# Kernel optimization log

Hardware: AMD Instinct MI355X
Metric: run time of the kernel (lower is better)

Reference implementation:

```python
import jax, jax.numpy as jnp
import numpy as np

B, S, D, H, W = 8, 2048, 128, 8, 64
INT_HEADS = 8          # hardcoded in SpatioTemporalLayer1
EPS_COS = 1e-8
EPS_LN = 1e-5


def _mha(q_in, k_in, v_in, in_w, in_b, out_w, out_b, nh, mask=None):
    # q_in/k_in/v_in: (batch, len, d); torch nn.MultiheadAttention math (eval, no dropout)
    b, lq, d = q_in.shape
    hd = d // nh
    q = (q_in @ in_w[:d].T + in_b[:d]).reshape(b, lq, nh, hd)
    k = (k_in @ in_w[d:2 * d].T + in_b[d:2 * d]).reshape(b, k_in.shape[1], nh, hd)
    v = (v_in @ in_w[2 * d:].T + in_b[2 * d:]).reshape(b, v_in.shape[1], nh, hd)
    scores = jnp.einsum('bihd,bjhd->bhij', q, k) / jnp.sqrt(jnp.asarray(hd, q_in.dtype))
    if mask is not None:
        scores = scores + mask
    attn = jax.nn.softmax(scores, axis=-1)
    out = jnp.einsum('bhij,bjhd->bihd', attn, v).reshape(b, lq, d)
    return out @ out_w.T + out_b


def _layernorm(x, g, b):
    mu = x.mean(-1, keepdims=True)
    var = ((x - mu) ** 2).mean(-1, keepdims=True)
    return (x - mu) * jax.lax.rsqrt(var + EPS_LN) * g + b


def _cos_normalize(e):
    n = jnp.maximum(jnp.linalg.norm(e, axis=-1, keepdims=True), EPS_COS)
    return e / n


def _forward(x, spatial_info, temporal_info,
             lw_in_w, lw_in_b, lw_out_w, lw_out_b,
             spat_w, spat_b, temp_w, temp_b,
             int_in_w, int_in_b, int_out_w, int_out_b,
             ffn_w1, ffn_b1, ffn_w2, ffn_b2,
             ln1_g, ln1_b, ln2_g, ln2_b):
    b, s, d = x.shape
    # --- local window attention (S % W == 0 here, so no padding path) ---
    nw = s // W
    xw = x.reshape(b * nw, W, d)
    causal = jnp.triu(jnp.full((W, W), -jnp.inf, x.dtype), k=1)
    attn = _mha(xw, xw, xw, lw_in_w, lw_in_b, lw_out_w, lw_out_b, H, causal).reshape(b, s, d)
    x = _layernorm(attn + x, ln1_g, ln1_b)
    # --- FFN (torch nn.GELU default = exact erf) ---
    h = jax.nn.gelu(x @ ffn_w1.T + ffn_b1, approximate=False)
    x = _layernorm(h @ ffn_w2.T + ffn_b2 + x, ln2_g, ln2_b)
    # --- spatio-temporal interaction ---
    se = spatial_info @ spat_w.T + spat_b
    te = temporal_info @ temp_w.T + temp_b
    sn = _cos_normalize(se)
    tn = _cos_normalize(te)
    ss = jnp.einsum('bid,bjd->bij', sn, sn)   # (B,S,S) spatial cosine sim
    ts = jnp.einsum('bid,bjd->bij', tn, tn)   # (B,S,S) temporal cosine sim
    # interaction MHA is batch_first=False: it treats (B,S,D) as (len=B, batch=S, d).
    # Equivalent batch-first call on swapped axes (faithful to the torch source).
    inter = jnp.swapaxes(
        _mha(jnp.swapaxes(se, 0, 1), jnp.swapaxes(te, 0, 1), jnp.swapaxes(te, 0, 1),
             int_in_w, int_in_b, int_out_w, int_out_b, INT_HEADS), 0, 1)
    # similarity[b,i,j,d] = ss[b,i,j]*ts[b,i,j]*inter[b,i,d]; mean over j factorizes:
    sim = (ss * ts).mean(axis=2)              # (B,S)
    return x + sim[..., None] * inter


def setup_inputs() -> dict:
    key = jax.random.key(0)
    ks = jax.random.split(key, 24)
    sc = 0.02
    inp = {
        'x': jax.random.normal(ks[0], (B, S, D), jnp.float32),
        'spatial_info': jax.random.normal(ks[1], (B, S, D), jnp.float32),
        'temporal_info': jax.random.normal(ks[2], (B, S, D), jnp.float32),
        'lw_in_w': jax.random.normal(ks[3], (3 * D, D), jnp.float32) * sc,
        'lw_in_b': jnp.zeros((3 * D,), jnp.float32),
        'lw_out_w': jax.random.normal(ks[4], (D, D), jnp.float32) * sc,
        'lw_out_b': jnp.zeros((D,), jnp.float32),
        'spat_w': jax.random.normal(ks[5], (D, D), jnp.float32) * sc,
        'spat_b': jnp.zeros((D,), jnp.float32),
        'temp_w': jax.random.normal(ks[6], (D, D), jnp.float32) * sc,
        'temp_b': jnp.zeros((D,), jnp.float32),
        'int_in_w': jax.random.normal(ks[7], (3 * D, D), jnp.float32) * sc,
        'int_in_b': jnp.zeros((3 * D,), jnp.float32),
        'int_out_w': jax.random.normal(ks[8], (D, D), jnp.float32) * sc,
        'int_out_b': jnp.zeros((D,), jnp.float32),
        'ffn_w1': jax.random.normal(ks[9], (4 * D, D), jnp.float32) * sc,
        'ffn_b1': jnp.zeros((4 * D,), jnp.float32),
        'ffn_w2': jax.random.normal(ks[10], (D, 4 * D), jnp.float32) * sc,
        'ffn_b2': jnp.zeros((D,), jnp.float32),
        'ln1_g': jnp.ones((D,), jnp.float32),
        'ln1_b': jnp.zeros((D,), jnp.float32),
        'ln2_g': jnp.ones((D,), jnp.float32),
        'ln2_b': jnp.zeros((D,), jnp.float32),
    }
    return inp


def reference(x, spatial_info, temporal_info,
              lw_in_w, lw_in_b, lw_out_w, lw_out_b,
              spat_w, spat_b, temp_w, temp_b,
              int_in_w, int_in_b, int_out_w, int_out_b,
              ffn_w1, ffn_b1, ffn_w2, ffn_b2,
              ln1_g, ln1_b, ln2_g, ln2_b):
    return _forward(x, spatial_info, temporal_info,
                    lw_in_w, lw_in_b, lw_out_w, lw_out_b,
                    spat_w, spat_b, temp_w, temp_b,
                    int_in_w, int_in_b, int_out_w, int_out_b,
                    ffn_w1, ffn_b1, ffn_w2, ffn_b2,
                    ln1_g, ln1_b, ln2_g, ln2_b)
```

## Files before the change

kernel.cpp:

```cpp
#include <hip/hip_runtime.h>
#include <math.h>

#define BB 8
#define SS 2048
#define NTOK (BB * SS)
#define ATB_SPLIT 16

using bf16x8 = __attribute__((ext_vector_type(8))) short;
using f32x4  = __attribute__((ext_vector_type(4))) float;

__device__ __forceinline__ float gelu_tanh(float x) {
    float y = 0.7978845608f * (x + 0.044715f * x * x * x);
    float e = __expf(2.0f * y);
    float t = 1.0f - 2.0f / (e + 1.0f);
    return 0.5f * x * (1.0f + t);
}
__device__ __forceinline__ unsigned short f2b(float f) {
    unsigned int u = __float_as_uint(f);
    u += 0x7FFFu + ((u >> 16) & 1u);
    return (unsigned short)(u >> 16);
}
__device__ __forceinline__ float b2f(unsigned short u) {
    return __uint_as_float((unsigned int)u << 16);
}
__device__ __forceinline__ bf16x8 ldg_f32_b8(const float* p) {
    float4 f0 = *(const float4*)p, f1 = *(const float4*)(p + 4);
    union { ushort4 u[2]; bf16x8 v; } r;
    r.u[0] = (ushort4){f2b(f0.x), f2b(f0.y), f2b(f0.z), f2b(f0.w)};
    r.u[1] = (ushort4){f2b(f1.x), f2b(f1.y), f2b(f1.z), f2b(f1.w)};
    return r.v;
}

__global__ __launch_bounds__(256) void phaseA(
    const float* __restrict__ x,
    const float* __restrict__ lw_in_w, const float* __restrict__ b_in,
    const float* __restrict__ lw_out_w, const float* __restrict__ b_out,
    const float* __restrict__ lng, const float* __restrict__ lnb,
    float* __restrict__ x1, unsigned short* __restrict__ x1b,
    const float* __restrict__ ffn_w1, const float* __restrict__ ffn_w2,
    unsigned short* __restrict__ Wb)
{
    __shared__ unsigned short Qs[64 * 136];
    __shared__ unsigned short Ks[64 * 136];
    __shared__ unsigned short Vt[128 * 72];
    __shared__ unsigned short Pb[4][32 * 72];
    __shared__ float red[2][64][2];
    const int tid = threadIdx.x;

    if (blockIdx.x >= 256) {
        int i = (blockIdx.x - 256) * 256 + tid;
        float v = (i < 65536) ? ffn_w1[i] : ffn_w2[i - 65536];
        Wb[i] = f2b(v);
        return;
    }

    const int m0 = blockIdx.x * 64;
    const int wv = tid >> 6, lane = tid & 63, ln = lane & 15, q = lane >> 4;
    const int wm = (wv >> 1) * 32, wn = (wv & 1) * 64;

    bf16x8 afr[4][2];
    #pragma unroll
    for (int kf = 0; kf < 4; ++kf)
        #pragma unroll
        for (int fm = 0; fm < 2; ++fm)
            afr[kf][fm] = ldg_f32_b8(x + (size_t)(m0 + wm + fm * 16 + ln) * 128 + kf * 32 + q * 8);

    #pragma unroll
    for (int p = 0; p < 3; ++p) {
        f32x4 acc[2][4] = {};
        #pragma unroll
        for (int kf = 0; kf < 4; ++kf) {
            bf16x8 b[4];
            #pragma unroll
            for (int fn = 0; fn < 4; ++fn)
                b[fn] = ldg_f32_b8(lw_in_w + (size_t)(p * 128 + wn + fn * 16 + ln) * 128 + kf * 32 + q * 8);
            #pragma unroll
            for (int fm = 0; fm < 2; ++fm)
                #pragma unroll
                for (int fn = 0; fn < 4; ++fn)
                    acc[fm][fn] = __builtin_amdgcn_mfma_f32_16x16x32_bf16(afr[kf][fm], b[fn], acc[fm][fn], 0, 0, 0);
        }
        #pragma unroll
        for (int fm = 0; fm < 2; ++fm)
            #pragma unroll
            for (int r = 0; r < 4; ++r) {
                int rl = wm + fm * 16 + q * 4 + r;
                #pragma unroll
                for (int fn = 0; fn < 4; ++fn) {
                    int col = wn + fn * 16 + ln;
                    unsigned short v = f2b(acc[fm][fn][r] + b_in[p * 128 + col]);
                    if (p == 0)      Qs[rl * 136 + col] = v;
                    else if (p == 1) Ks[rl * 136 + col] = v;
                    else             Vt[col * 72 + rl] = v;
                }
            }
    }
    __syncthreads();

    {
        const int mh = wv >> 1, hq = wv & 1;
        unsigned short* P = &Pb[wv][0];
        #pragma unroll
        for (int hh = 0; hh < 4; ++hh) {
            const int h = hq * 4 + hh;
            f32x4 sacc[2][4] = {};
            bf16x8 az[2] = {}, bz[4] = {};
            if (q < 2) {
                #pragma unroll
                for (int fm = 0; fm < 2; ++fm)
                    az[fm] = *(const bf16x8*)&Qs[(mh * 32 + fm * 16 + ln) * 136 + h * 16 + q * 8];
                #pragma unroll
                for (int fn = 0; fn < 4; ++fn)
                    bz[fn] = *(const bf16x8*)&Ks[(fn * 16 + ln) * 136 + h * 16 + q * 8];
            }
            #pragma unroll
            for (int fm = 0; fm < 2; ++fm)
                #pragma unroll
                for (int fn = 0; fn < 4; ++fn)
                    sacc[fm][fn] = __builtin_amdgcn_mfma_f32_16x16x32_bf16(az[fm], bz[fn], sacc[fm][fn], 0, 0, 0);
            float invr[2][4];
            #pragma unroll
            for (int fm = 0; fm < 2; ++fm)
                #pragma unroll
                for (int r = 0; r < 4; ++r) {
                    int gi = mh * 32 + fm * 16 + q * 4 + r;
                    float mx = -1e30f;
                    #pragma unroll
                    for (int fn = 0; fn < 4; ++fn) {
                        int j = fn * 16 + ln;
                        float s = sacc[fm][fn][r] * 0.25f;
                        if (j > gi) s = -1e30f;
                        sacc[fm][fn][r] = s;
                        mx = fmaxf(mx, s);
                    }
                    #pragma unroll
                    for (int off = 1; off < 16; off <<= 1)
                        mx = fmaxf(mx, __shfl_xor(mx, off, 64));
                    float sum = 0.0f;
                    #pragma unroll
                    for (int fn = 0; fn < 4; ++fn) {
                        float p_ = __expf(sacc[fm][fn][r] - mx);
                        sacc[fm][fn][r] = p_;
                        sum += p_;
                    }
                    #pragma unroll
                    for (int off = 1; off < 16; off <<= 1)
                        sum += __shfl_xor(sum, off, 64);
                    invr[fm][r] = 1.0f / sum;
                    #pragma unroll
                    for (int fn = 0; fn < 4; ++fn)
                        P[(fm * 16 + q * 4 + r) * 72 + fn * 16 + ln] = f2b(sacc[fm][fn][r]);
                }
            f32x4 oacc[2] = {};
            #pragma unroll
            for (int kf2 = 0; kf2 < 2; ++kf2) {
                bf16x8 pa[2], vb;
                #pragma unroll
                for (int fm = 0; fm < 2; ++fm)
                    pa[fm] = *(const bf16x8*)&P[(fm * 16 + ln) * 72 + kf2 * 32 + q * 8];
                vb = *(const bf16x8*)&Vt[(h * 16 + ln) * 72 + kf2 * 32 + q * 8];
                #pragma unroll
                for (int fm = 0; fm < 2; ++fm)
                    oacc[fm] = __builtin_amdgcn_mfma_f32_16x16x32_bf16(pa[fm], vb, oacc[fm], 0, 0, 0);
            }
            #pragma unroll
            for (int fm = 0; fm < 2; ++fm)
                #pragma unroll
                for (int r = 0; r < 4; ++r)
                    Qs[(mh * 32 + fm * 16 + q * 4 + r) * 136 + h * 16 + ln] =
                        f2b(oacc[fm][r] * invr[fm][r]);
        }
    }
    __syncthreads();

    f32x4 acc[2][4] = {};
    #pragma unroll
    for (int kf = 0; kf < 4; ++kf) {
        bf16x8 a[2], b[4];
        #pragma unroll
        for (int fm = 0; fm < 2; ++fm)
            a[fm] = *(const bf16x8*)&Qs[(wm + fm * 16 + ln) * 136 + kf * 32 + q * 8];
        #pragma unroll
        for (int fn = 0; fn < 4; ++fn)
            b[fn] = ldg_f32_b8(lw_out_w + (size_t)(wn + fn * 16 + ln) * 128 + kf * 32 + q * 8);
        #pragma unroll
        for (int fm = 0; fm < 2; ++fm)
            #pragma unroll
            for (int fn = 0; fn < 4; ++fn)
                acc[fm][fn] = __builtin_amdgcn_mfma_f32_16x16x32_bf16(a[fm], b[fn], acc[fm][fn], 0, 0, 0);
    }
    #pragma unroll
    for (int fm = 0; fm < 2; ++fm)
        #pragma unroll
        for (int r = 0; r < 4; ++r) {
            int rl = wm + fm * 16 + q * 4 + r;
            int row = m0 + rl;
            float s1 = 0.0f, s2 = 0.0f;
            #pragma unroll
            for (int fn = 0; fn < 4; ++fn) {
                int col = wn + fn * 16 + ln;
                float vv = acc[fm][fn][r] + b_out[col] + x[(size_t)row * 128 + col];
                acc[fm][fn][r] = vv;
                s1 += vv; s2 += vv * vv;
            }
            #pragma unroll
            for (int off = 1; off < 16; off <<= 1) {
                s1 += __shfl_xor(s1, off, 64);
                s2 += __shfl_xor(s2, off, 64);
            }
            if (ln == 0) { red[0][rl][wv & 1] = s1; red[1][rl][wv & 1] = s2; }
        }
    __syncthreads();
    #pragma unroll
    for (int fm = 0; fm < 2; ++fm)
        #pragma unroll
        for (int r = 0; r < 4; ++r) {
            int rl = wm + fm * 16 + q * 4 + r;
            int row = m0 + rl;
            float mu = (red[0][rl][0] + red[0][rl][1]) * (1.0f / 128.0f);
            float var = (red[1][rl][0] + red[1][rl][1]) * (1.0f / 128.0f) - mu * mu;
            float rs = rsqrtf(var + 1e-5f);
            #pragma unroll
            for (int fn = 0; fn < 4; ++fn) {
                int col = wn + fn * 16 + ln;
                float o = (acc[fm][fn][r] - mu) * rs * lng[col] + lnb[col];
                x1[(size_t)row * 128 + col] = o;
                x1b[(size_t)row * 128 + col] = f2b(o);
            }
        }
}

__global__ __launch_bounds__(256) void phaseB(
    const unsigned short* __restrict__ x1b, const float* __restrict__ x1,
    const unsigned short* __restrict__ Wb,
    const float* __restrict__ b1, const float* __restrict__ b2,
    const float* __restrict__ lng, const float* __restrict__ lnb,
    float* __restrict__ x2,
    const float* __restrict__ spatial, const float* __restrict__ temporal,
    const float* __restrict__ spat_w, const float* __restrict__ temp_w,
    const float* __restrict__ bsp, const float* __restrict__ btp,
    unsigned short* __restrict__ snb, unsigned short* __restrict__ tnb,
    unsigned short* __restrict__ seb, unsigned short* __restrict__ teb)
{
    __shared__ unsigned short Xs[32 * 136];
    __shared__ unsigned short Hs[32 * 72];
    __shared__ float redf[2][32][2];
    __shared__ float redp[64][2];
    const int tid = threadIdx.x;
    const int wv = tid >> 6, lane = tid & 63, ln = lane & 15, q = lane >> 4;

    if (blockIdx.x < 512) {
        const int t0 = blockIdx.x * 32;
        const int wm = (wv >> 1) * 16;
        const int wn1 = (wv & 1) * 32, wn2 = (wv & 1) * 64;
        const unsigned short* w1 = Wb;
        const unsigned short* w2 = Wb + 65536;

        const uint4* X4 = (const uint4*)(x1b + (size_t)t0 * 128);
        #pragma unroll
        for (int t = 0; t < 2; ++t) {
            int idx = tid + t * 256;
            int r = idx >> 4, c = idx & 15;
            *(uint4*)&Xs[r * 136 + c * 8] = X4[r * 16 + c];
        }
        __syncthreads();
        bf16x8 xfr[4];
        #pragma unroll
        for (int kf = 0; kf < 4; ++kf)
            xfr[kf] = *(const bf16x8*)&Xs[(wm + ln) * 136 + kf * 32 + q * 8];

        f32x4 acc2[4] = {};
        for (int ch = 0; ch < 8; ++ch) {
            const int hc0 = ch * 64;
            f32x4 acc1[2] = {};
            #pragma unroll
            for (int kf = 0; kf < 4; ++kf) {
                #pragma unroll
                for (int fn = 0; fn < 2; ++fn) {
                    bf16x8 bb = *(const bf16x8*)&w1[(size_t)(hc0 + wn1 + fn * 16 + ln) * 128 + kf * 32 + q * 8];
                    acc1[fn] = __builtin_amdgcn_mfma_f32_16x16x32_bf16(xfr[kf], bb, acc1[fn], 0, 0, 0);
                }
            }
            #pragma unroll
            for (int fn = 0; fn < 2; ++fn)
                #pragma unroll
                for (int r = 0; r < 4; ++r) {
                    int rl = wm + q * 4 + r;
                    int col = wn1 + fn * 16 + ln;
                    Hs[rl * 72 + col] = f2b(gelu_tanh(acc1[fn][r] + b1[hc0 + col]));
                }
            __syncthreads();
            #pragma unroll
            for (int kf2 = 0; kf2 < 2; ++kf2) {
                bf16x8 a = *(const bf16x8*)&Hs[(wm + ln) * 72 + kf2 * 32 + q * 8];
                #pragma unroll
                for (int fn = 0; fn < 4; ++fn) {
                    bf16x8 bb = *(const bf16x8*)&w2[(size_t)(wn2 + fn * 16 + ln) * 512 + hc0 + kf2 * 32 + q * 8];
                    acc2[fn] = __builtin_amdgcn_mfma_f32_16x16x32_bf16(a, bb, acc2[fn], 0, 0, 0);
                }
            }
            __syncthreads();
        }
        #pragma unroll
        for (int r = 0; r < 4; ++r) {
            int rl = wm + q * 4 + r;
            int row = t0 + rl;
            float s1 = 0.0f, s2 = 0.0f;
            #pragma unroll
            for (int fn = 0; fn < 4; ++fn) {
                int col = wn2 + fn * 16 + ln;
                float vv = acc2[fn][r] + b2[col] + x1[(size_t)row * 128 + col];
                acc2[fn][r] = vv;
                s1 += vv; s2 += vv * vv;
            }
            #pragma unroll
            for (int off = 1; off < 16; off <<= 1) {
                s1 += __shfl_xor(s1, off, 64);
                s2 += __shfl_xor(s2, off, 64);
            }
            if (ln == 0) { redf[0][rl][wv & 1] = s1; redf[1][rl][wv & 1] = s2; }
        }
        __syncthreads();
        #pragma unroll
        for (int r = 0; r < 4; ++r) {
            int rl = wm + q * 4 + r;
            int row = t0 + rl;
            float mu = (redf[0][rl][0] + redf[0][rl][1]) * (1.0f / 128.0f);
            float var = (redf[1][rl][0] + redf[1][rl][1]) * (1.0f / 128.0f) - mu * mu;
            float rs = rsqrtf(var + 1e-5f);
            #pragma unroll
            for (int fn = 0; fn < 4; ++fn) {
                int col = wn2 + fn * 16 + ln;
                x2[(size_t)row * 128 + col] = (acc2[fn][r] - mu) * rs * lng[col] + lnb[col];
            }
        }
        return;
    }

    {
        const int idx2 = blockIdx.x - 512;
        const int y = idx2 >> 8;
        const int m0 = (idx2 & 255) * 64;
        const float* Af = y ? temporal : spatial;
        const float* Wf = y ? temp_w : spat_w;
        const float* bias = y ? btp : bsp;
        unsigned short* nb = y ? tnb : snb;
        unsigned short* raw = y ? teb : seb;
        const int wm = (wv >> 1) * 32, wn = (wv & 1) * 64;

        f32x4 acc[2][4] = {};
        #pragma unroll
        for (int kf = 0; kf < 4; ++kf) {
            bf16x8 a[2], b[4];
            #pragma unroll
            for (int fm = 0; fm < 2; ++fm)
                a[fm] = ldg_f32_b8(Af + (size_t)(m0 + wm + fm * 16 + ln) * 128 + kf * 32 + q * 8);
            #pragma unroll
            for (int fn = 0; fn < 4; ++fn)
                b[fn] = ldg_f32_b8(Wf + (size_t)(wn + fn * 16 + ln) * 128 + kf * 32 + q * 8);
            #pragma unroll
            for (int fm = 0; fm < 2; ++fm)
                #pragma unroll
                for (int fn = 0; fn < 4; ++fn)
                    acc[fm][fn] = __builtin_amdgcn_mfma_f32_16x16x32_bf16(a[fm], b[fn], acc[fm][fn], 0, 0, 0);
        }
        #pragma unroll
        for (int fm = 0; fm < 2; ++fm)
            #pragma unroll
            for (int r = 0; r < 4; ++r) {
                int rl = wm + fm * 16 + q * 4 + r;
                float s2 = 0.0f;
                #pragma unroll
                for (int fn = 0; fn < 4; ++fn) {
                    int col = wn + fn * 16 + ln;
                    float vv = acc[fm][fn][r] + bias[col];
                    acc[fm][fn][r] = vv;
                    s2 += vv * vv;
                }
                #pragma unroll
                for (int off = 1; off < 16; off <<= 1) s2 += __shfl_xor(s2, off, 64);
                if (ln == 0) redp[rl][wv & 1] = s2;
            }
        __syncthreads();
        #pragma unroll
        for (int fm = 0; fm < 2; ++fm)
            #pragma unroll
            for (int r = 0; r < 4; ++r) {
                int rl = wm + fm * 16 + q * 4 + r;
                int row = m0 + rl;
                float inv = 1.0f / fmaxf(sqrtf(redp[rl][0] + redp[rl][1]), 1e-8f);
                #pragma unroll
                for (int fn = 0; fn < 4; ++fn) {
                    int col = wn + fn * 16 + ln;
                    float vv = acc[fm][fn][r];
                    nb[(size_t)row * 128 + col] = f2b(vv * inv);
                    raw[(size_t)row * 128 + col] = f2b(vv);
                }
            }
    }
}

__global__ __launch_bounds__(256) void atb_split_kernel(
    const unsigned short* __restrict__ snb, const unsigned short* __restrict__ tnb,
    float* __restrict__ part)
{
    const int b = blockIdx.z / ATB_SPLIT;
    const int chunk = blockIdx.z % ATB_SPLIT;
    const int d0 = blockIdx.x * 64, e0 = blockIdx.y * 64;
    __shared__ float Ss[32][68];
    __shared__ float Ts[32][68];
    const int tid = threadIdx.x;
    const int tx = tid % 16, ty = tid / 16;
    const int jbase = chunk * (SS / ATB_SPLIT);
    float acc[4][4] = {};
    for (int j0 = jbase; j0 < jbase + SS / ATB_SPLIT; j0 += 32) {
        {
            int r = tid >> 3, c8 = (tid & 7) * 8;
            uint4 sv = *(const uint4*)&snb[(size_t)(b * SS + j0 + r) * 128 + d0 + c8];
            uint4 tv = *(const uint4*)&tnb[(size_t)(b * SS + j0 + r) * 128 + e0 + c8];
            const unsigned short* sp = (const unsigned short*)&sv;
            const unsigned short* tp = (const unsigned short*)&tv;
            #pragma unroll
            for (int c = 0; c < 8; ++c) {
                Ss[r][c8 + c] = b2f(sp[c]);
                Ts[r][c8 + c] = b2f(tp[c]);
            }
        }
        __syncthreads();
        #pragma unroll
        for (int kk = 0; kk < 32; ++kk) {
            float4 af = *(const float4*)&Ss[kk][ty * 4];
            float4 wf = *(const float4*)&Ts[kk][tx * 4];
            float a[4] = {af.x, af.y, af.z, af.w};
            float w[4] = {wf.x, wf.y, wf.z, wf.w};
            #pragma unroll
            for (int i = 0; i < 4; ++i)
                #pragma unroll
                for (int j = 0; j < 4; ++j)
                    acc[i][j] = fmaf(a[i], w[j], acc[i][j]);
        }
        __syncthreads();
    }
    float* pp = part + (size_t)(b * ATB_SPLIT + chunk) * 16384;
    #pragma unroll
    for (int i = 0; i < 4; ++i) {
        float4 ov = {acc[i][0], acc[i][1], acc[i][2], acc[i][3]};
        *(float4*)&pp[(size_t)(d0 + ty * 4 + i) * 128 + e0 + tx * 4] = ov;
    }
}

__global__ __launch_bounds__(256) void atb_reduce_kernel(
    const float* __restrict__ part, unsigned short* __restrict__ Mtb)
{
    int i = blockIdx.x * 256 + threadIdx.x;
    int b = i >> 14, rem = i & 16383;
    int e = rem >> 7, d = rem & 127;
    const float* pp = part + (size_t)b * ATB_SPLIT * 16384 + (size_t)d * 128 + e;
    float s = 0.0f;
    #pragma unroll
    for (int c = 0; c < ATB_SPLIT; ++c) s += pp[(size_t)c * 16384];
    Mtb[i] = f2b(s);
}

__global__ __launch_bounds__(256) void simgemm_kernel(
    const unsigned short* __restrict__ snb, const unsigned short* __restrict__ tnb,
    const unsigned short* __restrict__ Mtb, float* __restrict__ sim)
{
    __shared__ float red[64][2];
    const int tid = threadIdx.x, m0 = blockIdx.x * 64, b = m0 >> 11;
    const int wv = tid >> 6, lane = tid & 63, ln = lane & 15, q = lane >> 4;
    const int wm = (wv >> 1) * 32, wn = (wv & 1) * 64;

    f32x4 acc[2][4] = {};
    #pragma unroll
    for (int kf = 0; kf < 4; ++kf) {
        bf16x8 a[2], bb[4];
        #pragma unroll
        for (int fm = 0; fm < 2; ++fm)
            a[fm] = *(const bf16x8*)&snb[(size_t)(m0 + wm + fm * 16 + ln) * 128 + kf * 32 + q * 8];
        #pragma unroll
        for (int fn = 0; fn < 4; ++fn)
            bb[fn] = *(const bf16x8*)&Mtb[(size_t)b * 16384 + (size_t)(wn + fn * 16 + ln) * 128 + kf * 32 + q * 8];
        #pragma unroll
        for (int fm = 0; fm < 2; ++fm)
            #pragma unroll
            for (int fn = 0; fn < 4; ++fn)
                acc[fm][fn] = __builtin_amdgcn_mfma_f32_16x16x32_bf16(a[fm], bb[fn], acc[fm][fn], 0, 0, 0);
    }
    #pragma unroll
    for (int fm = 0; fm < 2; ++fm)
        #pragma unroll
        for (int r = 0; r < 4; ++r) {
            int rl = wm + fm * 16 + q * 4 + r;
            int row = m0 + rl;
            float s = 0.0f;
            #pragma unroll
            for (int fn = 0; fn < 4; ++fn) {
                int col = wn + fn * 16 + ln;
                s += acc[fm][fn][r] * b2f(tnb[(size_t)row * 128 + col]);
            }
            #pragma unroll
            for (int off = 1; off < 16; off <<= 1) s += __shfl_xor(s, off, 64);
            if (ln == 0) red[rl][wv & 1] = s;
        }
    __syncthreads();
    if (tid < 64) sim[m0 + tid] = (red[tid][0] + red[tid][1]) * (1.0f / (float)SS);
}

__global__ __launch_bounds__(256) void inter_block(
    const unsigned short* __restrict__ seb, const unsigned short* __restrict__ teb,
    const float* __restrict__ Wint,
    const float* __restrict__ b_int,
    const float* __restrict__ Wio,
    const float* __restrict__ b_io,
    const float* __restrict__ sim, const float* __restrict__ x2,
    float* __restrict__ out)
{
    __shared__ unsigned short Qs[64 * 136];
    __shared__ unsigned short KVs[64 * 256];
    const int tid = threadIdx.x, s0 = blockIdx.x * 8;
    const int wv = tid >> 6, lane = tid & 63, ln = lane & 15, q = lane >> 4;
    const int wm = (wv >> 1) * 32, wn = (wv & 1) * 64;

    bf16x8 afr[4][2];
    #pragma unroll
    for (int kf = 0; kf < 4; ++kf)
        #pragma unroll
        for (int fm = 0; fm < 2; ++fm) {
            int rl = wm + fm * 16 + ln;
            size_t g = (size_t)(rl >> 3) * 2048 + s0 + (rl & 7);
            afr[kf][fm] = *(const bf16x8*)&seb[g * 128 + kf * 32 + q * 8];
        }

    #pragma unroll
    for (int p = 0; p < 3; ++p) {
        if (p == 1) {
            #pragma unroll
            for (int kf = 0; kf < 4; ++kf)
                #pragma unroll
                for (int fm = 0; fm < 2; ++fm) {
                    int rl = wm + fm * 16 + ln;
                    size_t g = (size_t)(rl >> 3) * 2048 + s0 + (rl & 7);
                    afr[kf][fm] = *(const bf16x8*)&teb[g * 128 + kf * 32 + q * 8];
                }
        }
        f32x4 acc[2][4] = {};
        #pragma unroll
        for (int kf = 0; kf < 4; ++kf) {
            bf16x8 b[4];
            #pragma unroll
            for (int fn = 0; fn < 4; ++fn)
                b[fn] = ldg_f32_b8(Wint + (size_t)(p * 128 + wn + fn * 16 + ln) * 128 + kf * 32 + q * 8);
            #pragma unroll
            for (int fm = 0; fm < 2; ++fm)
                #pragma unroll
                for (int fn = 0; fn < 4; ++fn)
                    acc[fm][fn] = __builtin_amdgcn_mfma_f32_16x16x32_bf16(afr[kf][fm], b[fn], acc[fm][fn], 0, 0, 0);
        }
        #pragma unroll
        for (int fm = 0; fm < 2; ++fm)
            #pragma unroll
            for (int r = 0; r < 4; ++r) {
                int rl = wm + fm * 16 + q * 4 + r;
                #pragma unroll
                for (int fn = 0; fn < 4; ++fn) {
                    int col = wn + fn * 16 + ln;
                    unsigned short v = f2b(acc[fm][fn][r] + b_int[p * 128 + col]);
                    if (p == 0) Qs[rl * 136 + col] = v;
                    else        KVs[rl * 256 + (p - 1) * 128 + col] = v;
                }
            }
        __syncthreads();
    }

    #pragma unroll
    for (int tt = 0; tt < 2; ++tt) {
        int task = tid + tt * 256;
        int ss = task >> 6, h = (task >> 3) & 7, i = task & 7;
        int rq = i * 8 + ss;
        float qr[16];
        {
            uint4 q0 = *(const uint4*)&Qs[rq * 136 + h * 16];
            uint4 q1 = *(const uint4*)&Qs[rq * 136 + h * 16 + 8];
            const unsigned short* p0 = (const unsigned short*)&q0;
            const unsigned short* p1 = (const unsigned short*)&q1;
            #pragma unroll
            for (int c = 0; c < 8; ++c) { qr[c] = b2f(p0[c]); qr[8 + c] = b2f(p1[c]); }
        }
        float sc[8];
        #pragma unroll
        for (int j = 0; j < 8; ++j) {
            uint4 k0 = *(const uint4*)&KVs[(j * 8 + ss) * 256 + h * 16];
            uint4 k1 = *(const uint4*)&KVs[(j * 8 + ss) * 256 + h * 16 + 8];
            const unsigned short* kp0 = (const unsigned short*)&k0;
            const unsigned short* kp1 = (const unsigned short*)&k1;
            float s = 0.0f;
            #pragma unroll
            for (int c = 0; c < 8; ++c) {
                s = fmaf(qr[c], b2f(kp0[c]), s);
                s = fmaf(qr[8 + c], b2f(kp1[c]), s);
            }
            sc[j] = s * 0.25f;
        }
        float mx = -1e30f;
        #pragma unroll
        for (int j = 0; j < 8; ++j) mx = fmaxf(mx, sc[j]);
        float pe[8], se = 0.0f;
        #pragma unroll
        for (int j = 0; j < 8; ++j) { pe[j] = __expf(sc[j] - mx); se += pe[j]; }
        float inv = 1.0f / se;
        float o[16] = {};
        #pragma unroll
        for (int j = 0; j < 8; ++j) {
            uint4 v0 = *(const uint4*)&KVs[(j * 8 + ss) * 256 + 128 + h * 16];
            uint4 v1 = *(const uint4*)&KVs[(j * 8 + ss) * 256 + 128 + h * 16 + 8];
            const unsigned short* vp0 = (const unsigned short*)&v0;
            const unsigned short* vp1 = (const unsigned short*)&v1;
            #pragma unroll
            for (int c = 0; c < 8; ++c) {
                o[c]     += pe[j] * b2f(vp0[c]);
                o[8 + c] += pe[j] * b2f(vp1[c]);
            }
        }
        ushort4 w0 = (ushort4){f2b(o[0]*inv),  f2b(o[1]*inv),  f2b(o[2]*inv),  f2b(o[3]*inv)};
        ushort4 w1 = (ushort4){f2b(o[4]*inv),  f2b(o[5]*inv),  f2b(o[6]*inv),  f2b(o[7]*inv)};
        ushort4 w2 = (ushort4){f2b(o[8]*inv),  f2b(o[9]*inv),  f2b(o[10]*inv), f2b(o[11]*inv)};
        ushort4 w3 = (ushort4){f2b(o[12]*inv), f2b(o[13]*inv), f2b(o[14]*inv), f2b(o[15]*inv)};
        *(ushort4*)&Qs[rq * 136 + h * 16]      = w0;
        *(ushort4*)&Qs[rq * 136 + h * 16 + 4]  = w1;
        *(ushort4*)&Qs[rq * 136 + h * 16 + 8]  = w2;
        *(ushort4*)&Qs[rq * 136 + h * 16 + 12] = w3;
    }
    __syncthreads();

    f32x4 acc[2][4] = {};
    #pragma unroll
    for (int kf = 0; kf < 4; ++kf) {
        bf16x8 a[2], b[4];
        #pragma unroll
        for (int fm = 0; fm < 2; ++fm)
            a[fm] = *(const bf16x8*)&Qs[(wm + fm * 16 + ln) * 136 + kf * 32 + q * 8];
        #pragma unroll
        for (int fn = 0; fn < 4; ++fn)
            b[fn] = ldg_f32_b8(Wio + (size_t)(wn + fn * 16 + ln) * 128 + kf * 32 + q * 8);
        #pragma unroll
        for (int fm = 0; fm < 2; ++fm)
            #pragma unroll
            for (int fn = 0; fn < 4; ++fn)
                acc[fm][fn] = __builtin_amdgcn_mfma_f32_16x16x32_bf16(a[fm], b[fn], acc[fm][fn], 0, 0, 0);
    }
    #pragma unroll
    for (int fm = 0; fm < 2; ++fm)
        #pragma unroll
        for (int r = 0; r < 4; ++r) {
            int rl = wm + fm * 16 + q * 4 + r;
            size_t g = (size_t)(rl >> 3) * 2048 + s0 + (rl & 7);
            float sc = sim[g];
            #pragma unroll
            for (int fn = 0; fn < 4; ++fn) {
                int col = wn + fn * 16 + ln;
                out[g * 128 + col] = (acc[fm][fn][r] + b_io[col]) * sc + x2[g * 128 + col];
            }
        }
}

extern "C" void kernel_launch(void* const* d_in, const int* in_sizes, int n_in,
                              void* d_out, int out_size, void* d_ws, size_t ws_size,
                              hipStream_t stream)
{
    const float* x        = (const float*)d_in[0];
    const float* spatial  = (const float*)d_in[1];
    const float* temporal = (const float*)d_in[2];
    const float* lw_in_w  = (const float*)d_in[3];
    const float* lw_in_b  = (const float*)d_in[4];
    const float* lw_out_w = (const float*)d_in[5];
    const float* lw_out_b = (const float*)d_in[6];
    const float* spat_w   = (const float*)d_in[7];
    const float* spat_b   = (const float*)d_in[8];
    const float* temp_w   = (const float*)d_in[9];
    const float* temp_b   = (const float*)d_in[10];
    const float* int_in_w = (const float*)d_in[11];
    const float* int_in_b = (const float*)d_in[12];
    const float* int_out_w= (const float*)d_in[13];
    const float* int_out_b= (const float*)d_in[14];
    const float* ffn_w1   = (const float*)d_in[15];
    const float* ffn_b1   = (const float*)d_in[16];
    const float* ffn_w2   = (const float*)d_in[17];
    const float* ffn_b2   = (const float*)d_in[18];
    const float* ln1_g    = (const float*)d_in[19];
    const float* ln1_b    = (const float*)d_in[20];
    const float* ln2_g    = (const float*)d_in[21];
    const float* ln2_b    = (const float*)d_in[22];
    float* out = (float*)d_out;

    char* base = (char*)d_ws;
    float*          x1   = (float*)(base + 0);
    unsigned short* x1b  = (unsigned short*)(base + 8388608);
    float*          x2   = (float*)(base + 12582912);
    unsigned short* snb  = (unsigned short*)(base + 20971520);
    unsigned short* tnb  = (unsigned short*)(base + 25165824);
    unsigned short* seb  = (unsigned short*)(base + 29360128);
    unsigned short* teb  = (unsigned short*)(base + 33554432);
    unsigned short* Mtb  = (unsigned short*)(base + 37748736);
    float*          simb = (float*)(base + 38010880);
    unsigned short* Wb   = (unsigned short*)(base + 38076416);
    float*          part = x1;

    phaseA<<<768, 256, 0, stream>>>(
        x, lw_in_w, lw_in_b, lw_out_w, lw_out_b, ln1_g, ln1_b, x1, x1b,
        ffn_w1, ffn_w2, Wb);
    phaseB<<<1024, 256, 0, stream>>>(
        x1b, x1, Wb, ffn_b1, ffn_b2, ln2_g, ln2_b, x2,
        spatial, temporal, spat_w, temp_w, spat_b, temp_b,
        snb, tnb, seb, teb);
    atb_split_kernel<<<dim3(2, 2, 8 * ATB_SPLIT), 256, 0, stream>>>(snb, tnb, part);
    atb_reduce_kernel<<<512, 256, 0, stream>>>(part, Mtb);
    simgemm_kernel<<<256, 256, 0, stream>>>(snb, tnb, Mtb, simb);
    inter_block<<<2048 / 8, 256, 0, stream>>>(
        seb, teb, int_in_w, int_in_b, int_out_w, int_out_b, simb, x2, out);
}
```

Before: 247.9 us.

## Give each wave full rows in phaseB to remove block barriers

phaseB's FFN and projection branches are restructured so that each wave owns 16 full rows across all 128 output columns. The per-wave GELU staging buffer then needs no __syncthreads, and the LayerNorm and L2-norm reductions finish within a wave via shuffles instead of a shared-memory cross-wave combine. Each block now covers 64 rows, so the FFN grid halves and the launch drops from 1024 to 768 blocks. The trade-off is more accumulator registers per wave (8 fragments instead of 4) and weight reads that are no longer split across waves, which may lower occupancy.

```diff
diff --git a/kernel.cpp b/kernel.cpp
--- a/kernel.cpp
+++ b/kernel.cpp
@@ -242,161 +242,121 @@
     unsigned short* __restrict__ snb, unsigned short* __restrict__ tnb,
     unsigned short* __restrict__ seb, unsigned short* __restrict__ teb)
 {
-    __shared__ unsigned short Xs[32 * 136];
-    __shared__ unsigned short Hs[32 * 72];
-    __shared__ float redf[2][32][2];
-    __shared__ float redp[64][2];
+    __shared__ unsigned short HsP[4][16 * 72];
     const int tid = threadIdx.x;
     const int wv = tid >> 6, lane = tid & 63, ln = lane & 15, q = lane >> 4;
 
-    if (blockIdx.x < 512) {
-        const int t0 = blockIdx.x * 32;
-        const int wm = (wv >> 1) * 16;
-        const int wn1 = (wv & 1) * 32, wn2 = (wv & 1) * 64;
+    if (blockIdx.x < 256) {
+        const int r0 = blockIdx.x * 64 + wv * 16;
         const unsigned short* w1 = Wb;
         const unsigned short* w2 = Wb + 65536;
-
-        const uint4* X4 = (const uint4*)(x1b + (size_t)t0 * 128);
-        #pragma unroll
-        for (int t = 0; t < 2; ++t) {
-            int idx = tid + t * 256;
-            int r = idx >> 4, c = idx & 15;
-            *(uint4*)&Xs[r * 136 + c * 8] = X4[r * 16 + c];
-        }
-        __syncthreads();
-        bf16x8 xfr[4];
+        unsigned short* Hp = &HsP[wv][0];
+
+        bf16x8 xa[4];
         #pragma unroll
         for (int kf = 0; kf < 4; ++kf)
-            xfr[kf] = *(const bf16x8*)&Xs[(wm + ln) * 136 + kf * 32 + q * 8];
-
-        f32x4 acc2[4] = {};
+            xa[kf] = *(const bf16x8*)&x1b[(size_t)(r0 + ln) * 128 + kf * 32 + q * 8];
+
+        f32x4 acc2[8] = {};
+        #pragma unroll
         for (int ch = 0; ch < 8; ++ch) {
             const int hc0 = ch * 64;
-            f32x4 acc1[2] = {};
-            #pragma unroll
-            for (int kf = 0; kf < 4; ++kf) {
-                #pragma unroll
-                for (int fn = 0; fn < 2; ++fn) {
-                    bf16x8 bb = *(const bf16x8*)&w1[(size_t)(hc0 + wn1 + fn * 16 + ln) * 128 + kf * 32 + q * 8];
-                    acc1[fn] = __builtin_amdgcn_mfma_f32_16x16x32_bf16(xfr[kf], bb, acc1[fn], 0, 0, 0);
+            f32x4 acc1[4] = {};
+            #pragma unroll
+            for (int kf = 0; kf < 4; ++kf)
+                #pragma unroll
+                for (int fn = 0; fn < 4; ++fn) {
+                    bf16x8 bb = *(const bf16x8*)&w1[(size_t)(hc0 + fn * 16 + ln) * 128 + kf * 32 + q * 8];
+                    acc1[fn] = __builtin_amdgcn_mfma_f32_16x16x32_bf16(xa[kf], bb, acc1[fn], 0, 0, 0);
                 }
-            }
-            #pragma unroll
-            for (int fn = 0; fn < 2; ++fn)
+            #pragma unroll
+            for (int fn = 0; fn < 4; ++fn)
                 #pragma unroll
                 for (int r = 0; r < 4; ++r) {
-                    int rl = wm + q * 4 + r;
-                    int col = wn1 + fn * 16 + ln;
-                    Hs[rl * 72 + col] = f2b(gelu_tanh(acc1[fn][r] + b1[hc0 + col]));
+                    int col = fn * 16 + ln;
+                    Hp[(q * 4 + r) * 72 + col] = f2b(gelu_tanh(acc1[fn][r] + b1[hc0 + col]));
                 }
-            __syncthreads();
             #pragma unroll
             for (int kf2 = 0; kf2 < 2; ++kf2) {
-                bf16x8 a = *(const bf16x8*)&Hs[(wm + ln) * 72 + kf2 * 32 + q * 8];
-                #pragma unroll
-                for (int fn = 0; fn < 4; ++fn) {
-                    bf16x8 bb = *(const bf16x8*)&w2[(size_t)(wn2 + fn * 16 + ln) * 512 + hc0 + kf2 * 32 + q * 8];
-                    acc2[fn] = __builtin_amdgcn_mfma_f32_16x16x32_bf16(a, bb, acc2[fn], 0, 0, 0);
+                bf16x8 ha = *(const bf16x8*)&Hp[ln * 72 + kf2 * 32 + q * 8];
+                #pragma unroll
+                for (int fn = 0; fn < 8; ++fn) {
+                    bf16x8 bb = *(const bf16x8*)&w2[(size_t)(fn * 16 + ln) * 512 + hc0 + kf2 * 32 + q * 8];
+                    acc2[fn] = __builtin_amdgcn_mfma_f32_16x16x32_bf16(ha, bb, acc2[fn], 0, 0, 0);
                 }
             }
-            __syncthreads();
         }
         #pragma unroll
         for (int r = 0; r < 4; ++r) {
-            int rl = wm + q * 4 + r;
-            int row = t0 + rl;
+            int row = r0 + q * 4 + r;
             float s1 = 0.0f, s2 = 0.0f;
-            #pragma unroll
-            for (int fn = 0; fn < 4; ++fn) {
-                int col = wn2 + fn * 16 + ln;
-                float vv = acc2[fn][r] + b2[col] + x1[(size_t)row * 128 + col];
-                acc2[fn][r] = vv;
-                s1 += vv; s2 += vv * vv;
+            float vv[8];
+            #pragma unroll
+            for (int fn = 0; fn < 8; ++fn) {
+                int col = fn * 16 + ln;
+                vv[fn] = acc2[fn][r] + b2[col] + x1[(size_t)row * 128 + col];
+                s1 += vv[fn]; s2 += vv[fn] * vv[fn];
             }
             #pragma unroll
             for (int off = 1; off < 16; off <<= 1) {
                 s1 += __shfl_xor(s1, off, 64);
                 s2 += __shfl_xor(s2, off, 64);
             }
-            if (ln == 0) { redf[0][rl][wv & 1] = s1; redf[1][rl][wv & 1] = s2; }
-        }
-        __syncthreads();
-        #pragma unroll
-        for (int r = 0; r < 4; ++r) {
-            int rl = wm + q * 4 + r;
-            int row = t0 + rl;
-            float mu = (redf[0][rl][0] + redf[0][rl][1]) * (1.0f / 128.0f);
-            float var = (redf[1][rl][0] + redf[1][rl][1]) * (1.0f / 128.0f) - mu * mu;
+            float mu = s1 * (1.0f / 128.0f);
+            float var = s2 * (1.0f / 128.0f) - mu * mu;
             float rs = rsqrtf(var + 1e-5f);
             #pragma unroll
-            for (int fn = 0; fn < 4; ++fn) {
-                int col = wn2 + fn * 16 + ln;
-                x2[(size_t)row * 128 + col] = (acc2[fn][r] - mu) * rs * lng[col] + lnb[col];
+            for (int fn = 0; fn < 8; ++fn) {
+                int col = fn * 16 + ln;
+                x2[(size_t)row * 128 + col] = (vv[fn] - mu) * rs * lng[col] + lnb[col];
             }
         }
         return;
     }
 
     {
-        const int idx2 = blockIdx.x - 512;
+        const int idx2 = blockIdx.x - 256;
         const int y = idx2 >> 8;
-        const int m0 = (idx2 & 255) * 64;
+        const int r0 = (idx2 & 255) * 64 + wv * 16;
         const float* Af = y ? temporal : spatial;
         const float* Wf = y ? temp_w : spat_w;
         const float* bias = y ? btp : bsp;
         unsigned short* nb = y ? tnb : snb;
         unsigned short* raw = y ? teb : seb;
-        const int wm = (wv >> 1) * 32, wn = (wv & 1) * 64;
-
-        f32x4 acc[2][4] = {};
-        #pragma unroll
-        for (int kf = 0; kf < 4; ++kf) {
-            bf16x8 a[2], b[4];
-            #pragma unroll
-            for (int fm = 0; fm < 2; ++fm)
-                a[fm] = ldg_f32_b8(Af + (size_t)(m0 + wm + fm * 16 + ln) * 128 + kf * 32 + q * 8);
-            #pragma unroll
-            for (int fn = 0; fn < 4; ++fn)
-                b[fn] = ldg_f32_b8(Wf + (size_t)(wn + fn * 16 + ln) * 128 + kf * 32 + q * 8);
-            #pragma unroll
-            for (int fm = 0; fm < 2; ++fm)
-                #pragma unroll
-                for (int fn = 0; fn < 4; ++fn)
-                    acc[fm][fn] = __builtin_amdgcn_mfma_f32_16x16x32_bf16(a[fm], b[fn], acc[fm][fn], 0, 0, 0);
-        }
-        #pragma unroll
-        for (int fm = 0; fm < 2; ++fm)
-            #pragma unroll
-            for (int r = 0; r < 4; ++r) {
-                int rl = wm + fm * 16 + q * 4 + r;
-                float s2 = 0.0f;
-                #pragma unroll
-                for (int fn = 0; fn < 4; ++fn) {
-                    int col = wn + fn * 16 + ln;
-                    float vv = acc[fm][fn][r] + bias[col];
-                    acc[fm][fn][r] = vv;
-                    s2 += vv * vv;
-                }
-                #pragma unroll
-                for (int off = 1; off < 16; off <<= 1) s2 += __shfl_xor(s2, off, 64);
-                if (ln == 0) redp[rl][wv & 1] = s2;
-            }
-        __syncthreads();
-        #pragma unroll
-        for (int fm = 0; fm < 2; ++fm)
-            #pragma unroll
-            for (int r = 0; r < 4; ++r) {
-                int rl = wm + fm * 16 + q * 4 + r;
-                int row = m0 + rl;
-                float inv = 1.0f / fmaxf(sqrtf(redp[rl][0] + redp[rl][1]), 1e-8f);
-                #pragma unroll
-                for (int fn = 0; fn < 4; ++fn) {
-                    int col = wn + fn * 16 + ln;
-                    float vv = acc[fm][fn][r];
-                    nb[(size_t)row * 128 + col] = f2b(vv * inv);
-                    raw[(size_t)row * 128 + col] = f2b(vv);
-                }
-            }
+
+        bf16x8 a[4];
+        #pragma unroll
+        for (int kf = 0; kf < 4; ++kf)
+            a[kf] = ldg_f32_b8(Af + (size_t)(r0 + ln) * 128 + kf * 32 + q * 8);
+
+        f32x4 acc[8] = {};
+        #pragma unroll
+        for (int kf = 0; kf < 4; ++kf)
+            #pragma unroll
+            for (int fn = 0; fn < 8; ++fn) {
+                bf16x8 bb = ldg_f32_b8(Wf + (size_t)(fn * 16 + ln) * 128 + kf * 32 + q * 8);
+                acc[fn] = __builtin_amdgcn_mfma_f32_16x16x32_bf16(a[kf], bb, acc[fn], 0, 0, 0);
+            }
+        #pragma unroll
+        for (int r = 0; r < 4; ++r) {
+            int row = r0 + q * 4 + r;
+            float s2 = 0.0f;
+            float vv[8];
+            #pragma unroll
+            for (int fn = 0; fn < 8; ++fn) {
+                vv[fn] = acc[fn][r] + bias[fn * 16 + ln];
+                s2 += vv[fn] * vv[fn];
+            }
+            #pragma unroll
+            for (int off = 1; off < 16; off <<= 1) s2 += __shfl_xor(s2, off, 64);
+            float inv = 1.0f / fmaxf(sqrtf(s2), 1e-8f);
+            #pragma unroll
+            for (int fn = 0; fn < 8; ++fn) {
+                int col = fn * 16 + ln;
+                nb[(size_t)row * 128 + col] = f2b(vv[fn] * inv);
+                raw[(size_t)row * 128 + col] = f2b(vv[fn]);
+            }
+        }
     }
 }
 
@@ -709,7 +669,7 @@
     phaseA<<<768, 256, 0, stream>>>(
         x, lw_in_w, lw_in_b, lw_out_w, lw_out_b, ln1_g, ln1_b, x1, x1b,
         ffn_w1, ffn_w2, Wb);
-    phaseB<<<1024, 256, 0, stream>>>(
+    phaseB<<<768, 256, 0, stream>>>(
         x1b, x1, Wb, ffn_b1, ffn_b2, ln2_g, ln2_b, x2,
         spatial, temporal, spat_w, temp_w, spat_b, temp_b,
         snb, tnb, seb, teb);
```

New measurement: 286.9 us. 1.16x slower.

## Split phaseB into separate FFN and projection kernels with larger FFN row tiles

Applied to the files above, without the earlier changes.

The combined phaseB kernel is split into a dedicated fused FFN kernel and a separate spatio-temporal projection kernel. The FFN kernel now processes 64 tokens per block instead of 32, so each W1/W2 fragment loaded from global memory feeds twice as many MFMAs. The hidden tile is double-buffered in shared memory, which removes the second barrier per chunk. In exchange the FFN grid drops to 256 blocks with higher register and LDS use, and there is one extra kernel launch.

```diff
diff --git a/kernel.cpp b/kernel.cpp
--- a/kernel.cpp
+++ b/kernel.cpp
@@ -230,174 +230,186 @@
         }
 }
 
-__global__ __launch_bounds__(256) void phaseB(
+__global__ __launch_bounds__(256) void ffn_fused(
     const unsigned short* __restrict__ x1b, const float* __restrict__ x1,
-    const unsigned short* __restrict__ Wb,
+    const unsigned short* __restrict__ w1, const unsigned short* __restrict__ w2,
     const float* __restrict__ b1, const float* __restrict__ b2,
     const float* __restrict__ lng, const float* __restrict__ lnb,
-    float* __restrict__ x2,
-    const float* __restrict__ spatial, const float* __restrict__ temporal,
-    const float* __restrict__ spat_w, const float* __restrict__ temp_w,
+    float* __restrict__ x2)
+{
+    __shared__ unsigned short Xs[64 * 136];
+    __shared__ unsigned short Hs[2][64 * 72];
+    __shared__ float red[2][64][2];
+    const int tid = threadIdx.x, t0 = blockIdx.x * 64;
+    const int wv = tid >> 6, lane = tid & 63, ln = lane & 15, q = lane >> 4;
+    const int wm = (wv >> 1) * 32;
+    const int wn1 = (wv & 1) * 32, wn2 = (wv & 1) * 64;
+
+    const uint4* X4 = (const uint4*)(x1b + (size_t)t0 * 128);
+    #pragma unroll
+    for (int t = 0; t < 4; ++t) {
+        int idx = tid + t * 256;
+        int r = idx >> 4, c = idx & 15;
+        *(uint4*)&Xs[r * 136 + c * 8] = X4[r * 16 + c];
+    }
+    __syncthreads();
+
+    bf16x8 xfr[4][2];
+    #pragma unroll
+    for (int kf = 0; kf < 4; ++kf)
+        #pragma unroll
+        for (int fm = 0; fm < 2; ++fm)
+            xfr[kf][fm] = *(const bf16x8*)&Xs[(wm + fm * 16 + ln) * 136 + kf * 32 + q * 8];
+
+    f32x4 acc2[2][4] = {};
+    for (int ch = 0; ch < 8; ++ch) {
+        const int hc0 = ch * 64;
+        unsigned short* Hb = &Hs[ch & 1][0];
+        f32x4 acc1[2][2] = {};
+        #pragma unroll
+        for (int kf = 0; kf < 4; ++kf) {
+            bf16x8 b[2];
+            #pragma unroll
+            for (int fn = 0; fn < 2; ++fn)
+                b[fn] = *(const bf16x8*)&w1[(size_t)(hc0 + wn1 + fn * 16 + ln) * 128 + kf * 32 + q * 8];
+            #pragma unroll
+            for (int fm = 0; fm < 2; ++fm)
+                #pragma unroll
+                for (int fn = 0; fn < 2; ++fn)
+                    acc1[fm][fn] = __builtin_amdgcn_mfma_f32_16x16x32_bf16(xfr[kf][fm], b[fn], acc1[fm][fn], 0, 0, 0);
+        }
+        #pragma unroll
+        for (int fm = 0; fm < 2; ++fm)
+            #pragma unroll
+            for (int fn = 0; fn < 2; ++fn)
+                #pragma unroll
+                for (int r = 0; r < 4; ++r) {
+                    int rl = wm + fm * 16 + q * 4 + r;
+                    int col = wn1 + fn * 16 + ln;
+                    Hb[rl * 72 + col] = f2b(gelu_tanh(acc1[fm][fn][r] + b1[hc0 + col]));
+                }
+        __syncthreads();
+        #pragma unroll
+        for (int kf2 = 0; kf2 < 2; ++kf2) {
+            bf16x8 a[2], b[4];
+            #pragma unroll
+            for (int fm = 0; fm < 2; ++fm)
+                a[fm] = *(const bf16x8*)&Hb[(wm + fm * 16 + ln) * 72 + kf2 * 32 + q * 8];
+            #pragma unroll
+            for (int fn = 0; fn < 4; ++fn)
+                b[fn] = *(const bf16x8*)&w2[(size_t)(wn2 + fn * 16 + ln) * 512 + hc0 + kf2 * 32 + q * 8];
+            #pragma unroll
+            for (int fm = 0; fm < 2; ++fm)
+                #pragma unroll
+                for (int fn = 0; fn < 4; ++fn)
+                    acc2[fm][fn] = __builtin_amdgcn_mfma_f32_16x16x32_bf16(a[fm], b[fn], acc2[fm][fn], 0, 0, 0);
+        }
+    }
+    #pragma unroll
+    for (int fm = 0; fm < 2; ++fm)
+        #pragma unroll
+        for (int r = 0; r < 4; ++r) {
+            int rl = wm + fm * 16 + q * 4 + r;
+            int row = t0 + rl;
+            float s1 = 0.0f, s2 = 0.0f;
+            #pragma unroll
+            for (int fn = 0; fn < 4; ++fn) {
+                int col = wn2 + fn * 16 + ln;
+                float vv = acc2[fm][fn][r] + b2[col] + x1[(size_t)row * 128 + col];
+                acc2[fm][fn][r] = vv;
+                s1 += vv; s2 += vv * vv;
+            }
+            #pragma unroll
+            for (int off = 1; off < 16; off <<= 1) {
+                s1 += __shfl_xor(s1, off, 64);
+                s2 += __shfl_xor(s2, off, 64);
+            }
+            if (ln == 0) { red[0][rl][wv & 1] = s1; red[1][rl][wv & 1] = s2; }
+        }
+    __syncthreads();
+    #pragma unroll
+    for (int fm = 0; fm < 2; ++fm)
+        #pragma unroll
+        for (int r = 0; r < 4; ++r) {
+            int rl = wm + fm * 16 + q * 4 + r;
+            int row = t0 + rl;
+            float mu = (red[0][rl][0] + red[0][rl][1]) * (1.0f / 128.0f);
+            float var = (red[1][rl][0] + red[1][rl][1]) * (1.0f / 128.0f) - mu * mu;
+            float rs = rsqrtf(var + 1e-5f);
+            #pragma unroll
+            for (int fn = 0; fn < 4; ++fn) {
+                int col = wn2 + fn * 16 + ln;
+                x2[(size_t)row * 128 + col] = (acc2[fm][fn][r] - mu) * rs * lng[col] + lnb[col];
+            }
+        }
+}
+
+__global__ __launch_bounds__(256) void stproj_kernel(
+    const float* __restrict__ sp, const float* __restrict__ tp,
+    const float* __restrict__ Wsp, const float* __restrict__ Wtp,
     const float* __restrict__ bsp, const float* __restrict__ btp,
     unsigned short* __restrict__ snb, unsigned short* __restrict__ tnb,
     unsigned short* __restrict__ seb, unsigned short* __restrict__ teb)
 {
-    __shared__ unsigned short Xs[32 * 136];
-    __shared__ unsigned short Hs[32 * 72];
-    __shared__ float redf[2][32][2];
-    __shared__ float redp[64][2];
-    const int tid = threadIdx.x;
+    __shared__ float red[64][2];
+    const int tid = threadIdx.x, m0 = blockIdx.x * 64, y = blockIdx.y;
+    const float* Af = y ? tp : sp;
+    const float* Wf = y ? Wtp : Wsp;
+    const float* bias = y ? btp : bsp;
+    unsigned short* nb = y ? tnb : snb;
+    unsigned short* raw = y ? teb : seb;
     const int wv = tid >> 6, lane = tid & 63, ln = lane & 15, q = lane >> 4;
-
-    if (blockIdx.x < 512) {
-        const int t0 = blockIdx.x * 32;
-        const int wm = (wv >> 1) * 16;
-        const int wn1 = (wv & 1) * 32, wn2 = (wv & 1) * 64;
-        const unsigned short* w1 = Wb;
-        const unsigned short* w2 = Wb + 65536;
-
-        const uint4* X4 = (const uint4*)(x1b + (size_t)t0 * 128);
-        #pragma unroll
-        for (int t = 0; t < 2; ++t) {
-            int idx = tid + t * 256;
-            int r = idx >> 4, c = idx & 15;
-            *(uint4*)&Xs[r * 136 + c * 8] = X4[r * 16 + c];
-        }
-        __syncthreads();
-        bf16x8 xfr[4];
-        #pragma unroll
-        for (int kf = 0; kf < 4; ++kf)
-            xfr[kf] = *(const bf16x8*)&Xs[(wm + ln) * 136 + kf * 32 + q * 8];
-
-        f32x4 acc2[4] = {};
-        for (int ch = 0; ch < 8; ++ch) {
-            const int hc0 = ch * 64;
-            f32x4 acc1[2] = {};
-            #pragma unroll
-            for (int kf = 0; kf < 4; ++kf) {
-                #pragma unroll
-                for (int fn = 0; fn < 2; ++fn) {
-                    bf16x8 bb = *(const bf16x8*)&w1[(size_t)(hc0 + wn1 + fn * 16 + ln) * 128 + kf * 32 + q * 8];
-                    acc1[fn] = __builtin_amdgcn_mfma_f32_16x16x32_bf16(xfr[kf], bb, acc1[fn], 0, 0, 0);
-                }
-            }
-            #pragma unroll
-            for (int fn = 0; fn < 2; ++fn)
-                #pragma unroll
-                for (int r = 0; r < 4; ++r) {
-                    int rl = wm + q * 4 + r;
-                    int col = wn1 + fn * 16 + ln;
-                    Hs[rl * 72 + col] = f2b(gelu_tanh(acc1[fn][r] + b1[hc0 + col]));
-                }
-            __syncthreads();
-            #pragma unroll
-            for (int kf2 = 0; kf2 < 2; ++kf2) {
-                bf16x8 a = *(const bf16x8*)&Hs[(wm + ln) * 72 + kf2 * 32 + q * 8];
-                #pragma unroll
-                for (int fn = 0; fn < 4; ++fn) {
-                    bf16x8 bb = *(const bf16x8*)&w2[(size_t)(wn2 + fn * 16 + ln) * 512 + hc0 + kf2 * 32 + q * 8];
-                    acc2[fn] = __builtin_amdgcn_mfma_f32_16x16x32_bf16(a, bb, acc2[fn], 0, 0, 0);
-                }
-            }
-            __syncthreads();
-        }
+    const int wm = (wv >> 1) * 32, wn = (wv & 1) * 64;
+
+    f32x4 acc[2][4] = {};
+    #pragma unroll
+    for (int kf = 0; kf < 4; ++kf) {
+        bf16x8 a[2], b[4];
+        #pragma unroll
+        for (int fm = 0; fm < 2; ++fm)
+            a[fm] = ldg_f32_b8(Af + (size_t)(m0 + wm + fm * 16 + ln) * 128 + kf * 32 + q * 8);
+        #pragma unroll
+        for (int fn = 0; fn < 4; ++fn)
+            b[fn] = ldg_f32_b8(Wf + (size_t)(wn + fn * 16 + ln) * 128 + kf * 32 + q * 8);
+        #pragma unroll
+        for (int fm = 0; fm < 2; ++fm)
+            #pragma unroll
+            for (int fn = 0; fn < 4; ++fn)
+                acc[fm][fn] = __builtin_amdgcn_mfma_f32_16x16x32_bf16(a[fm], b[fn], acc[fm][fn], 0, 0, 0);
+    }
+    #pragma unroll
+    for (int fm = 0; fm < 2; ++fm)
         #pragma unroll
         for (int r = 0; r < 4; ++r) {
-            int rl = wm + q * 4 + r;
-            int row = t0 + rl;
-            float s1 = 0.0f, s2 = 0.0f;
+            int rl = wm + fm * 16 + q * 4 + r;
+            float s2 = 0.0f;
             #pragma unroll
             for (int fn = 0; fn < 4; ++fn) {
-                int col = wn2 + fn * 16 + ln;
-                float vv = acc2[fn][r] + b2[col] + x1[(size_t)row * 128 + col];
-                acc2[fn][r] = vv;
-                s1 += vv; s2 += vv * vv;
-            }
-            #pragma unroll
-            for (int off = 1; off < 16; off <<= 1) {
-                s1 += __shfl_xor(s1, off, 64);
-                s2 += __shfl_xor(s2, off, 64);
-            }
-            if (ln == 0) { redf[0][rl][wv & 1] = s1; redf[1][rl][wv & 1] = s2; }
-        }
-        __syncthreads();
+                int col = wn + fn * 16 + ln;
+                float vv = acc[fm][fn][r] + bias[col];
+                acc[fm][fn][r] = vv;
+                s2 += vv * vv;
+            }
+            #pragma unroll
+            for (int off = 1; off < 16; off <<= 1) s2 += __shfl_xor(s2, off, 64);
+            if (ln == 0) red[rl][wv & 1] = s2;
+        }
+    __syncthreads();
+    #pragma unroll
+    for (int fm = 0; fm < 2; ++fm)
         #pragma unroll
         for (int r = 0; r < 4; ++r) {
-            int rl = wm + q * 4 + r;
-            int row = t0 + rl;
-            float mu = (redf[0][rl][0] + redf[0][rl][1]) * (1.0f / 128.0f);
-            float var = (redf[1][rl][0] + redf[1][rl][1]) * (1.0f / 128.0f) - mu * mu;
-            float rs = rsqrtf(var + 1e-5f);
+            int rl = wm + fm * 16 + q * 4 + r;
+            int row = m0 + rl;
+            float inv = 1.0f / fmaxf(sqrtf(red[rl][0] + red[rl][1]), 1e-8f);
             #pragma unroll
             for (int fn = 0; fn < 4; ++fn) {
-                int col = wn2 + fn * 16 + ln;
-                x2[(size_t)row * 128 + col] = (acc2[fn][r] - mu) * rs * lng[col] + lnb[col];
-            }
-        }
-        return;
-    }
-
-    {
-        const int idx2 = blockIdx.x - 512;
-        const int y = idx2 >> 8;
-        const int m0 = (idx2 & 255) * 64;
-        const float* Af = y ? temporal : spatial;
-        const float* Wf = y ? temp_w : spat_w;
-        const float* bias = y ? btp : bsp;
-        unsigned short* nb = y ? tnb : snb;
-        unsigned short* raw = y ? teb : seb;
-        const int wm = (wv >> 1) * 32, wn = (wv & 1) * 64;
-
-        f32x4 acc[2][4] = {};
-        #pragma unroll
-        for (int kf = 0; kf < 4; ++kf) {
-            bf16x8 a[2], b[4];
-            #pragma unroll
-            for (int fm = 0; fm < 2; ++fm)
-                a[fm] = ldg_f32_b8(Af + (size_t)(m0 + wm + fm * 16 + ln) * 128 + kf * 32 + q * 8);
-            #pragma unroll
-            for (int fn = 0; fn < 4; ++fn)
-                b[fn] = ldg_f32_b8(Wf + (size_t)(wn + fn * 16 + ln) * 128 + kf * 32 + q * 8);
-            #pragma unroll
-            for (int fm = 0; fm < 2; ++fm)
-                #pragma unroll
-                for (int fn = 0; fn < 4; ++fn)
-                    acc[fm][fn] = __builtin_amdgcn_mfma_f32_16x16x32_bf16(a[fm], b[fn], acc[fm][fn], 0, 0, 0);
-        }
-        #pragma unroll
-        for (int fm = 0; fm < 2; ++fm)
-            #pragma unroll
-            for (int r = 0; r < 4; ++r) {
-                int rl = wm + fm * 16 + q * 4 + r;
-                float s2 = 0.0f;
-                #pragma unroll
-                for (int fn = 0; fn < 4; ++fn) {
-                    int col = wn + fn * 16 + ln;
-                    float vv = acc[fm][fn][r] + bias[col];
-                    acc[fm][fn][r] = vv;
-                    s2 += vv * vv;
-                }
-                #pragma unroll
-                for (int off = 1; off < 16; off <<= 1) s2 += __shfl_xor(s2, off, 64);
-                if (ln == 0) redp[rl][wv & 1] = s2;
-            }
-        __syncthreads();
-        #pragma unroll
-        for (int fm = 0; fm < 2; ++fm)
-            #pragma unroll
-            for (int r = 0; r < 4; ++r) {
-                int rl = wm + fm * 16 + q * 4 + r;
-                int row = m0 + rl;
-                float inv = 1.0f / fmaxf(sqrtf(redp[rl][0] + redp[rl][1]), 1e-8f);
-                #pragma unroll
-                for (int fn = 0; fn < 4; ++fn) {
-                    int col = wn + fn * 16 + ln;
-                    float vv = acc[fm][fn][r];
-                    nb[(size_t)row * 128 + col] = f2b(vv * inv);
-                    raw[(size_t)row * 128 + col] = f2b(vv);
-                }
-            }
-    }
+                int col = wn + fn * 16 + ln;
+                float vv = acc[fm][fn][r];
+                nb[(size_t)row * 128 + col] = f2b(vv * inv);
+                raw[(size_t)row * 128 + col] = f2b(vv);
+            }
+        }
 }
 
 __global__ __launch_bounds__(256) void atb_split_kernel(
@@ -709,8 +721,9 @@
     phaseA<<<768, 256, 0, stream>>>(
         x, lw_in_w, lw_in_b, lw_out_w, lw_out_b, ln1_g, ln1_b, x1, x1b,
         ffn_w1, ffn_w2, Wb);
-    phaseB<<<1024, 256, 0, stream>>>(
-        x1b, x1, Wb, ffn_b1, ffn_b2, ln2_g, ln2_b, x2,
+    ffn_fused<<<256, 256, 0, stream>>>(
+        x1b, x1, Wb, Wb + 65536, ffn_b1, ffn_b2, ln2_g, ln2_b, x2);
+    stproj_kernel<<<dim3(256, 2), 256, 0, stream>>>(
         spatial, temporal, spat_w, temp_w, spat_b, temp_b,
         snb, tnb, seb, teb);
     atb_split_kernel<<<dim3(2, 2, 8 * ATB_SPLIT), 256, 0, stream>>>(snb, tnb, part);
```

Result: no change. 249.3 us (+0.6%).
